# Performance work log

Measured on AMD Instinct MI355X. Metric: run time of the kernel, lower is better.

The kernel has to match this reference:

```python
import jax, jax.numpy as jnp
import numpy as np

G, S, P = 128, 32, 16          # graphs, subgraphs per graph, nodes per subgraph
D, C, NH, OUT = 768, 256, 4, 7 # input dim, hidden dim, GAT heads, classes


def setup_inputs() -> dict:
    key = jax.random.key(0)
    ks = jax.random.split(key, 17)
    n = lambda k, shape, s=0.05: jax.random.normal(k, shape, dtype=jnp.float32) * s
    return {
        "x": jax.random.normal(ks[0], (G, S, P, D), dtype=jnp.float32),
        # GATConv(768 -> 256, heads=4, concat=False): lin weight, att vectors, bias
        "gat_W": n(ks[1], (D, NH * C)),
        "att_src": n(ks[2], (NH, C)),
        "att_dst": n(ks[3], (NH, C)),
        "gat_b": n(ks[4], (C,)),
        # GRU(256 -> 256), torch layout [3*H, in]
        "gru_Wih": n(ks[5], (3 * C, C)),
        "gru_Whh": n(ks[6], (3 * C, C)),
        "gru_bih": n(ks[7], (3 * C,)),
        "gru_bhh": n(ks[8], (3 * C,)),
        # scale_up_projection Linear(256 -> 768)
        "up_W": n(ks[9], (D, C)),
        "up_b": n(ks[10], (D,)),
        # speaker_projection Linear(1536 -> 768) + ReLU
        "sp_W": n(ks[11], (D, 2 * D)),
        "sp_b": n(ks[12], (D,)),
        # GlobalAttention gate Linear(256 -> 1)
        "att_W": n(ks[13], (1, C)),
        "att_b": n(ks[14], (1,)),
        # classifier Linear(256 -> 7)
        "cls_W": n(ks[15], (OUT, C)),
        "cls_b": n(ks[16], (OUT,)),
    }


def _gat(x, W, a_src, a_dst, b):
    # PyG GATConv on a star graph (speaker = local node 0 -> all others) with
    # default add_self_loops=True, negative_slope=0.2, concat=False (mean over heads).
    # x: [G, P, D]
    h = jnp.einsum('gpd,dhc->gphc', x, W.reshape(D, NH, C))     # per-head transform
    es = jnp.sum(h * a_src, -1)                                 # [G, P, NH]
    ed = jnp.sum(h * a_dst, -1)
    lrelu = lambda v: jnp.where(v > 0, v, 0.2 * v)
    e_spk = lrelu(es[:, :1] + ed)   # edge speaker -> t
    e_slf = lrelu(es + ed)          # self loop t -> t
    w = jax.nn.softmax(jnp.stack([e_spk, e_slf], -1), axis=-1)  # [G, P, NH, 2]
    # for t == 0 both terms are h[:,0] and weights sum to 1, matching the
    # speaker node receiving only its self loop.
    out = w[..., 0:1] * h[:, :1] + w[..., 1:2] * h              # [G, P, NH, C]
    return out.mean(axis=2) + b


def _gru_cell(xin, h, Wih, Whh, bih, bhh):
    gi = xin @ Wih.T + bih
    gh = h @ Whh.T + bhh
    ir, iz, inn = jnp.split(gi, 3, -1)
    hr, hz, hn = jnp.split(gh, 3, -1)
    r = jax.nn.sigmoid(ir + hr)
    z = jax.nn.sigmoid(iz + hz)
    return (1 - z) * jnp.tanh(inn + r * hn) + z * h


def _forward(x, gat_W, att_src, att_dst, gat_b, gru_Wih, gru_Whh, gru_bih, gru_bhh,
             up_W, up_b, sp_W, sp_b, att_W, att_b, cls_W, cls_b):
    g, s, p, d = x.shape
    m0 = _gat(x[:, 0], gat_W, att_src, att_dst, gat_b)  # [G, P, C]
    h0 = jnp.zeros((g, p, C), x.dtype)

    def step(carry, _):
        h_run, m_prev = carry
        # running GRU hidden over memory prefix, then one zero-input step
        # (equivalent to rerunning the GRU over [m_0..m_{j-1}, 0])
        h_run = _gru_cell(m_prev, h_run, gru_Wih, gru_Whh, gru_bih, gru_bhh)
        h_nxt = _gru_cell(jnp.zeros_like(h_run), h_run, gru_Wih, gru_Whh, gru_bih, gru_bhh)
        pooled = h_nxt @ up_W.T + up_b                  # [G, P, D]
        # faithful to source: non_speaker_indices covers ALL nodes (torch.equal
        # shape-mismatch bug), and speaker_info is read AFTER the overwrite,
        # so the speaker concat is [pooled, pooled] and raw x[:, j>=1] is unused.
        spk = jnp.concatenate([pooled[:, 0], pooled[:, 0]], -1)  # [G, 2D]
        spk = jax.nn.relu(spk @ sp_W.T + sp_b)
        x_new = pooled.at[:, 0].set(spk)
        m = _gat(x_new, gat_W, att_src, att_dst, gat_b)
        return (h_run, m), m

    (_, _), ms = jax.lax.scan(step, (h0, m0), None, length=s - 1)
    mem = jnp.concatenate([m0[None], ms], axis=0)        # [S, G, P, C]
    # GlobalAttention pool over the P nodes of each subgraph memory state
    gate = jax.nn.softmax(jnp.squeeze(mem @ att_W.T + att_b, -1), axis=-1)  # [S, G, P]
    pooled = jnp.einsum('sgp,sgpc->sgc', gate, mem)
    logits = pooled @ cls_W.T + cls_b                    # [S, G, OUT]
    # torch stacks graph-major: [G*S, 1, OUT]
    return jnp.transpose(logits, (1, 0, 2)).reshape(g * s, 1, OUT)


def reference(x, gat_W, att_src, att_dst, gat_b, gru_Wih, gru_Whh, gru_bih, gru_bhh,
              up_W, up_b, sp_W, sp_b, att_W, att_b, cls_W, cls_b):
    return _forward(x, gat_W, att_src, att_dst, gat_b, gru_Wih, gru_Whh, gru_bih,
                    gru_bhh, up_W, up_b, sp_W, sp_b, att_W, att_b, cls_W, cls_b)
```

## Files before the change

kernel.cpp:

```cpp
#include <hip/hip_runtime.h>
#include <math.h>

#define NG 128
#define NS 32
#define NP 16
#define ND 768
#define NC 256
#define NHD 4
#define NOUT 7
#define NR 2048

typedef unsigned short ushortT;
typedef short bf16x8 __attribute__((ext_vector_type(8)));
typedef float f32x4 __attribute__((ext_vector_type(4)));

__device__ __forceinline__ ushortT f2b(float f) {
    union { float f; unsigned u; } v; v.f = f;
    unsigned r = (v.u + 0x7FFF + ((v.u >> 16) & 1)) >> 16;
    return (ushortT)r;
}
__device__ __forceinline__ float sigf(float v) { return 1.f / (1.f + expf(-v)); }

#define MFMA16(a, b, c) __builtin_amdgcn_mfma_f32_16x16x32_bf16((a), (b), (c), 0, 0, 0)

__global__ __launch_bounds__(256) void bgemm_kernel(
    const ushortT* __restrict__ A, const ushortT* __restrict__ Asub,
    const ushortT* __restrict__ Bt, const float* __restrict__ bias,
    float* __restrict__ outF, ushortT* __restrict__ outH,
    int N, int K, int act)
{
    __shared__ short As[64 * 40];
    __shared__ short Bs[64 * 40];
    const int tid = threadIdx.x;
    const int lane = tid & 63, wid = tid >> 6;
    const int quad = lane >> 4, l15 = lane & 15;
    const int row0 = blockIdx.y * 64, col0 = blockIdx.x * 64;
    const int mh = (wid & 1) * 32, nh = (wid >> 1) * 32;
    const int sr = tid >> 2, skq = (tid & 3) * 8;
    const int grow_s = row0 + sr;
    const ushortT* aptr = (Asub && ((grow_s & 15) == 0))
        ? Asub + (size_t)(grow_s >> 4) * K : A + (size_t)grow_s * K;
    const ushortT* bptr = Bt + (size_t)(col0 + sr) * K;

    f32x4 acc[2][2];
    for (int i = 0; i < 2; ++i)
        for (int j = 0; j < 2; ++j) acc[i][j] = (f32x4){0.f, 0.f, 0.f, 0.f};

    for (int kk = 0; kk < K; kk += 32) {
        __syncthreads();
        *(uint4*)&As[sr * 40 + skq] = *(const uint4*)(aptr + kk + skq);
        *(uint4*)&Bs[sr * 40 + skq] = *(const uint4*)(bptr + kk + skq);
        __syncthreads();
        bf16x8 af0 = *(const bf16x8*)&As[(mh + l15) * 40 + quad * 8];
        bf16x8 af1 = *(const bf16x8*)&As[(mh + 16 + l15) * 40 + quad * 8];
        bf16x8 bf0 = *(const bf16x8*)&Bs[(nh + l15) * 40 + quad * 8];
        bf16x8 bf1 = *(const bf16x8*)&Bs[(nh + 16 + l15) * 40 + quad * 8];
        acc[0][0] = MFMA16(af0, bf0, acc[0][0]);
        acc[0][1] = MFMA16(af0, bf1, acc[0][1]);
        acc[1][0] = MFMA16(af1, bf0, acc[1][0]);
        acc[1][1] = MFMA16(af1, bf1, acc[1][1]);
    }
#pragma unroll
    for (int mt = 0; mt < 2; ++mt)
#pragma unroll
        for (int nt = 0; nt < 2; ++nt) {
            const int gc = col0 + nh + nt * 16 + l15;
            const float bv = bias ? bias[gc] : 0.f;
#pragma unroll
            for (int r = 0; r < 4; ++r) {
                const int gr = row0 + mh + mt * 16 + quad * 4 + r;
                float v = acc[mt][nt][r] + bv;
                if (act) v = fmaxf(v, 0.f);
                if (outF) outF[(size_t)gr * N + gc] = v;
                if (outH) outH[(size_t)gr * N + gc] = f2b(v);
            }
        }
}

__global__ __launch_bounds__(256) void gru1_mfma_kernel(
    const ushortT* __restrict__ mB, const ushortT* __restrict__ hB,
    const ushortT* __restrict__ WihB, const ushortT* __restrict__ WhhB,
    const float* __restrict__ bih, const float* __restrict__ bhh,
    float* __restrict__ hF, ushortT* __restrict__ hBout)
{
    __shared__ short As[2 * 32 * 264];
    __shared__ short Bs[384 * 40];
    const int tid = threadIdx.x;
    const int lane = tid & 63, wid = tid >> 6;
    const int quad = lane >> 4, l15 = lane & 15;
    const int row0 = blockIdx.y * 32;
    const int n0 = blockIdx.x * 64;
    const int mt = wid & 1, nhh = (wid >> 1) * 32;

    for (int c = tid; c < 2048; c += 256) {
        const int mat = c >> 10, r2 = c & 1023, row = r2 >> 5, kc = (r2 & 31) * 8;
        const ushortT* src = (mat ? hB : mB) + (size_t)(row0 + row) * NC + kc;
        *(uint4*)&As[mat * 8448 + row * 264 + kc] = *(const uint4*)src;
    }
    f32x4 acc[2][3][2];
    for (int w = 0; w < 2; ++w)
        for (int g = 0; g < 3; ++g)
            for (int n = 0; n < 2; ++n) acc[w][g][n] = (f32x4){0.f, 0.f, 0.f, 0.f};

    for (int kk = 0; kk < 256; kk += 32) {
        __syncthreads();
        for (int c = tid; c < 1536; c += 256) {
            const int j = c >> 2, kq = (c & 3) * 8;
            const int w = j / 192, j2 = j - w * 192, gt = j2 >> 6, nloc = j2 & 63;
            const ushortT* src = (w ? WhhB : WihB) +
                (size_t)(gt * 256 + n0 + nloc) * NC + kk + kq;
            *(uint4*)&Bs[j * 40 + kq] = *(const uint4*)src;
        }
        __syncthreads();
        bf16x8 af0 = *(const bf16x8*)&As[(mt * 16 + l15) * 264 + kk + quad * 8];
        bf16x8 af1 = *(const bf16x8*)&As[8448 + (mt * 16 + l15) * 264 + kk + quad * 8];
#pragma unroll
        for (int gt = 0; gt < 3; ++gt)
#pragma unroll
            for (int nt = 0; nt < 2; ++nt) {
                const int jb = gt * 64 + nhh + nt * 16 + l15;
                bf16x8 b0 = *(const bf16x8*)&Bs[jb * 40 + quad * 8];
                bf16x8 b1 = *(const bf16x8*)&Bs[(192 + jb) * 40 + quad * 8];
                acc[0][gt][nt] = MFMA16(af0, b0, acc[0][gt][nt]);
                acc[1][gt][nt] = MFMA16(af1, b1, acc[1][gt][nt]);
            }
    }
#pragma unroll
    for (int nt = 0; nt < 2; ++nt) {
        const int c = n0 + nhh + nt * 16 + l15;
        const float br = bih[c], bz = bih[256 + c], bn = bih[512 + c];
        const float cr = bhh[c], cz = bhh[256 + c], cn = bhh[512 + c];
#pragma unroll
        for (int r = 0; r < 4; ++r) {
            const int grow = row0 + mt * 16 + quad * 4 + r;
            const size_t idx = (size_t)grow * NC + c;
            const float hold = hF[idx];
            const float rg = sigf(acc[0][0][nt][r] + br + acc[1][0][nt][r] + cr);
            const float zg = sigf(acc[0][1][nt][r] + bz + acc[1][1][nt][r] + cz);
            const float ng = tanhf(acc[0][2][nt][r] + bn + rg * (acc[1][2][nt][r] + cn));
            const float hn = (1.f - zg) * ng + zg * hold;
            hF[idx] = hn;
            hBout[idx] = f2b(hn);
        }
    }
}

__global__ __launch_bounds__(256) void gru2_mfma_kernel(
    const ushortT* __restrict__ hB, const ushortT* __restrict__ WhhB,
    const float* __restrict__ bih, const float* __restrict__ bhh,
    const float* __restrict__ hF, ushortT* __restrict__ hnB,
    ushortT* __restrict__ h0c)
{
    __shared__ short As[32 * 264];
    __shared__ short Bs[192 * 40];
    const int tid = threadIdx.x;
    const int lane = tid & 63, wid = tid >> 6;
    const int quad = lane >> 4, l15 = lane & 15;
    const int row0 = blockIdx.y * 32;
    const int n0 = blockIdx.x * 64;
    const int mt = wid & 1, nhh = (wid >> 1) * 32;

    for (int c = tid; c < 1024; c += 256) {
        const int row = c >> 5, kc = (c & 31) * 8;
        *(uint4*)&As[row * 264 + kc] =
            *(const uint4*)(hB + (size_t)(row0 + row) * NC + kc);
    }
    f32x4 acc[3][2];
    for (int g = 0; g < 3; ++g)
        for (int n = 0; n < 2; ++n) acc[g][n] = (f32x4){0.f, 0.f, 0.f, 0.f};

    for (int kk = 0; kk < 256; kk += 32) {
        __syncthreads();
        for (int c = tid; c < 768; c += 256) {
            const int j = c >> 2, kq = (c & 3) * 8;
            const int gt = j >> 6, nloc = j & 63;
            *(uint4*)&Bs[j * 40 + kq] =
                *(const uint4*)(WhhB + (size_t)(gt * 256 + n0 + nloc) * NC + kk + kq);
        }
        __syncthreads();
        bf16x8 af = *(const bf16x8*)&As[(mt * 16 + l15) * 264 + kk + quad * 8];
#pragma unroll
        for (int gt = 0; gt < 3; ++gt)
#pragma unroll
            for (int nt = 0; nt < 2; ++nt) {
                const int jb = gt * 64 + nhh + nt * 16 + l15;
                bf16x8 b = *(const bf16x8*)&Bs[jb * 40 + quad * 8];
                acc[gt][nt] = MFMA16(af, b, acc[gt][nt]);
            }
    }
#pragma unroll
    for (int nt = 0; nt < 2; ++nt) {
        const int c = n0 + nhh + nt * 16 + l15;
        const float br = bih[c], bz = bih[256 + c], bn = bih[512 + c];
        const float cr = bhh[c], cz = bhh[256 + c], cn = bhh[512 + c];
#pragma unroll
        for (int r = 0; r < 4; ++r) {
            const int grow = row0 + mt * 16 + quad * 4 + r;
            const size_t idx = (size_t)grow * NC + c;
            const float rg = sigf(br + acc[0][nt][r] + cr);
            const float zg = sigf(bz + acc[1][nt][r] + cz);
            const float ng = tanhf(bn + rg * (acc[2][nt][r] + cn));
            const float hv = (1.f - zg) * ng + zg * hF[idx];
            const ushortT hb = f2b(hv);
            hnB[idx] = hb;
            if ((grow & 15) == 0) h0c[(size_t)(grow >> 4) * NC + c] = hb;
        }
    }
}

__global__ __launch_bounds__(256) void fin_kernel(
    const float* __restrict__ hbuf, const float* __restrict__ att_src,
    const float* __restrict__ att_dst, const float* __restrict__ gat_b,
    const float* __restrict__ attW, const float* __restrict__ attb,
    const float* __restrict__ clsW, const float* __restrict__ clsb,
    ushortT* __restrict__ mB, float* __restrict__ outp, int s)
{
    const int g = blockIdx.x, tid = threadIdx.x;
    const int lane = tid & 63, wid = tid >> 6;
    __shared__ float es_s[16][4], ed_s[16][4];
    __shared__ float m_s[16][260];
    __shared__ float gate_s[16];
    __shared__ float pooled_s[256];
    const float* hb = hbuf + (size_t)g * NP * (NHD * NC);

    for (int pi = 0; pi < 4; ++pi) {
        const int p = wid * 4 + pi;
        const float* row = hb + p * (NHD * NC);
        float ss[4] = {0.f, 0.f, 0.f, 0.f}, sd[4] = {0.f, 0.f, 0.f, 0.f};
#pragma unroll
        for (int i = 0; i < 16; ++i) {
            const int col = lane + 64 * i;
            const float v = row[col];
            ss[i >> 2] += v * att_src[col];
            sd[i >> 2] += v * att_dst[col];
        }
        for (int off = 32; off; off >>= 1)
#pragma unroll
            for (int h = 0; h < 4; ++h) {
                ss[h] += __shfl_down(ss[h], off);
                sd[h] += __shfl_down(sd[h], off);
            }
        if (lane == 0)
#pragma unroll
            for (int h = 0; h < 4; ++h) { es_s[p][h] = ss[h]; ed_s[p][h] = sd[h]; }
    }
    __syncthreads();
    {
        const int p = tid >> 4, cb = (tid & 15) * 16;
        float accv[16];
#pragma unroll
        for (int cj = 0; cj < 16; ++cj) accv[cj] = 0.f;
#pragma unroll
        for (int h = 0; h < 4; ++h) {
            float e1 = es_s[0][h] + ed_s[p][h]; e1 = e1 > 0.f ? e1 : 0.2f * e1;
            float e2 = es_s[p][h] + ed_s[p][h]; e2 = e2 > 0.f ? e2 : 0.2f * e2;
            const float mx = fmaxf(e1, e2);
            float w0 = expf(e1 - mx), w1 = expf(e2 - mx);
            const float inv = 1.f / (w0 + w1);
            w0 *= inv; w1 *= inv;
            const float* r0 = hb + h * NC + cb;
            const float* rp = hb + p * (NHD * NC) + h * NC + cb;
#pragma unroll
            for (int cj = 0; cj < 16; ++cj) accv[cj] += w0 * r0[cj] + w1 * rp[cj];
        }
#pragma unroll
        for (int cj = 0; cj < 16; ++cj) {
            const float v = accv[cj] * 0.25f + gat_b[cb + cj];
            m_s[p][cb + cj] = v;
            mB[(size_t)(g * NP + p) * NC + cb + cj] = f2b(v);
        }
    }
    __syncthreads();
    for (int pi = 0; pi < 4; ++pi) {
        const int p = wid * 4 + pi;
        float sg = 0.f;
#pragma unroll
        for (int i = 0; i < 4; ++i) { const int c = lane + 64 * i; sg += m_s[p][c] * attW[c]; }
        for (int off = 32; off; off >>= 1) sg += __shfl_down(sg, off);
        if (lane == 0) gate_s[p] = sg + attb[0];
    }
    __syncthreads();
    float mx = -1e30f;
#pragma unroll
    for (int p = 0; p < 16; ++p) mx = fmaxf(mx, gate_s[p]);
    float ge[16], ssum = 0.f;
#pragma unroll
    for (int p = 0; p < 16; ++p) { ge[p] = expf(gate_s[p] - mx); ssum += ge[p]; }
    const float inv = 1.f / ssum;
    {
        float pc = 0.f;
#pragma unroll
        for (int p = 0; p < 16; ++p) pc += ge[p] * m_s[p][tid];
        pooled_s[tid] = pc * inv;
    }
    __syncthreads();
    const int o = tid >> 5, l32 = tid & 31;
    if (o < NOUT) {
        float a = 0.f;
#pragma unroll
        for (int i = 0; i < 8; ++i) {
            const int c = l32 + 32 * i;
            a += pooled_s[c] * clsW[o * NC + c];
        }
        for (int off = 16; off; off >>= 1) a += __shfl_down(a, off);
        if (l32 == 0) outp[((size_t)g * NS + s) * NOUT + o] = a + clsb[o];
    }
}

__global__ __launch_bounds__(256) void cast_kernel(const float* __restrict__ a,
                                                   ushortT* __restrict__ b, int n) {
    const int i = blockIdx.x * 256 + threadIdx.x;
    if (i < n) b[i] = f2b(a[i]);
}
__global__ __launch_bounds__(256) void gatT_kernel(const float* __restrict__ gW,
                                                   ushortT* __restrict__ gB) {
    const int idx = blockIdx.x * 256 + threadIdx.x;
    const int c = idx / ND, d = idx - c * ND;
    gB[idx] = f2b(gW[(size_t)d * (NHD * NC) + c]);
}
__global__ __launch_bounds__(256) void spwc_kernel(const float* __restrict__ spW,
                                                   float* __restrict__ o) {
    const int idx = blockIdx.x * 256 + threadIdx.x;
    const int r = idx / ND, d = idx - r * ND;
    o[idx] = spW[(size_t)r * (2 * ND) + d] + spW[(size_t)r * (2 * ND) + ND + d];
}
__global__ __launch_bounds__(256) void wus_kernel(const float* __restrict__ spWc,
                                                  const float* __restrict__ upW,
                                                  ushortT* __restrict__ WusB) {
    const int c = threadIdx.x;
    const int o0 = blockIdx.x * 16;
    float acc[16];
#pragma unroll
    for (int i = 0; i < 16; ++i) acc[i] = 0.f;
    for (int d = 0; d < ND; ++d) {
        const float u = upW[(size_t)d * NC + c];
#pragma unroll
        for (int i = 0; i < 16; ++i) acc[i] += spWc[(size_t)(o0 + i) * ND + d] * u;
    }
#pragma unroll
    for (int i = 0; i < 16; ++i) WusB[(size_t)(o0 + i) * NC + c] = f2b(acc[i]);
}
__global__ __launch_bounds__(256) void bus_kernel(const float* __restrict__ spWc,
                                                  const float* __restrict__ up_b,
                                                  const float* __restrict__ sp_b,
                                                  float* __restrict__ bus) {
    const int o = blockIdx.x * 256 + threadIdx.x;
    if (o >= ND) return;
    float a = sp_b[o];
    const float* sr = spWc + (size_t)o * ND;
    for (int d = 0; d < ND; ++d) a += sr[d] * up_b[d];
    bus[o] = a;
}
__global__ __launch_bounds__(256) void x0_kernel(const float* __restrict__ x,
                                                 ushortT* __restrict__ xb) {
    const int idx = blockIdx.x * 256 + threadIdx.x;
    const int row = idx / ND, d = idx - row * ND;
    const int g = row >> 4, p = row & 15;
    xb[idx] = f2b(x[((size_t)g * (NS * NP) + p) * ND + d]);
}
__global__ __launch_bounds__(256) void zh_kernel(float* hF, ushortT* hB) {
    const int idx = blockIdx.x * 256 + threadIdx.x;
    hF[idx] = 0.f;
    hB[idx] = 0;
}

extern "C" void kernel_launch(void* const* d_in, const int* in_sizes, int n_in,
                              void* d_out, int out_size, void* d_ws, size_t ws_size,
                              hipStream_t stream) {
    (void)in_sizes; (void)n_in; (void)out_size; (void)ws_size;
    const float* x       = (const float*)d_in[0];
    const float* gat_W   = (const float*)d_in[1];
    const float* att_src = (const float*)d_in[2];
    const float* att_dst = (const float*)d_in[3];
    const float* gat_b   = (const float*)d_in[4];
    const float* gru_Wih = (const float*)d_in[5];
    const float* gru_Whh = (const float*)d_in[6];
    const float* gru_bih = (const float*)d_in[7];
    const float* gru_bhh = (const float*)d_in[8];
    const float* up_W    = (const float*)d_in[9];
    const float* up_b    = (const float*)d_in[10];
    const float* sp_W    = (const float*)d_in[11];
    const float* sp_b    = (const float*)d_in[12];
    const float* att_W   = (const float*)d_in[13];
    const float* att_b   = (const float*)d_in[14];
    const float* cls_W   = (const float*)d_in[15];
    const float* cls_b   = (const float*)d_in[16];
    float* outp = (float*)d_out;

    char* w = (char*)d_ws;
    ushortT* xb    = (ushortT*)w; w += (size_t)NR * ND * 2;
    ushortT* WihB  = (ushortT*)w; w += (size_t)(3 * NC) * NC * 2;
    ushortT* WhhB  = (ushortT*)w; w += (size_t)(3 * NC) * NC * 2;
    ushortT* upWB  = (ushortT*)w; w += (size_t)ND * NC * 2;
    ushortT* gatB  = (ushortT*)w; w += (size_t)(NHD * NC) * ND * 2;
    ushortT* WusB  = (ushortT*)w; w += (size_t)ND * NC * 2;
    float*   spWc  = (float*)w;   w += (size_t)ND * ND * 4;
    float*   bus   = (float*)w;   w += (size_t)ND * 4;
    float*   hF    = (float*)w;   w += (size_t)NR * NC * 4;
    ushortT* hB    = (ushortT*)w; w += (size_t)NR * NC * 2;
    ushortT* hnB   = (ushortT*)w; w += (size_t)NR * NC * 2;
    ushortT* h0c   = (ushortT*)w; w += (size_t)NG * NC * 2;
    ushortT* poolB = (ushortT*)w; w += (size_t)NR * ND * 2;
    ushortT* spkB  = (ushortT*)w; w += (size_t)NG * ND * 2;
    float*   hbuf  = (float*)w;   w += (size_t)NR * (NHD * NC) * 4;
    ushortT* mB    = (ushortT*)w; w += (size_t)NR * NC * 2;

    cast_kernel<<<768, 256, 0, stream>>>(gru_Wih, WihB, 3 * NC * NC);
    cast_kernel<<<768, 256, 0, stream>>>(gru_Whh, WhhB, 3 * NC * NC);
    cast_kernel<<<768, 256, 0, stream>>>(up_W, upWB, ND * NC);
    gatT_kernel<<<(NHD * NC * ND) / 256, 256, 0, stream>>>(gat_W, gatB);
    spwc_kernel<<<(ND * ND) / 256, 256, 0, stream>>>(sp_W, spWc);
    wus_kernel<<<ND / 16, 256, 0, stream>>>(spWc, up_W, WusB);
    bus_kernel<<<3, 256, 0, stream>>>(spWc, up_b, sp_b, bus);
    x0_kernel<<<(NR * ND) / 256, 256, 0, stream>>>(x, xb);
    zh_kernel<<<(NR * NC) / 256, 256, 0, stream>>>(hF, hB);

    bgemm_kernel<<<dim3((NHD * NC) / 64, NR / 64), 256, 0, stream>>>(
        xb, nullptr, gatB, nullptr, hbuf, nullptr, NHD * NC, ND, 0);
    fin_kernel<<<NG, 256, 0, stream>>>(hbuf, att_src, att_dst, gat_b,
                                       att_W, att_b, cls_W, cls_b, mB, outp, 0);

    for (int j = 1; j < NS; ++j) {
        gru1_mfma_kernel<<<dim3(NC / 64, NR / 32), 256, 0, stream>>>(
            mB, hB, WihB, WhhB, gru_bih, gru_bhh, hF, hB);
        gru2_mfma_kernel<<<dim3(NC / 64, NR / 32), 256, 0, stream>>>(
            hB, WhhB, gru_bih, gru_bhh, hF, hnB, h0c);
        bgemm_kernel<<<dim3(ND / 64, NR / 64), 256, 0, stream>>>(
            hnB, nullptr, upWB, up_b, nullptr, poolB, ND, NC, 0);
        bgemm_kernel<<<dim3(ND / 64, NG / 64), 256, 0, stream>>>(
            h0c, nullptr, WusB, bus, nullptr, spkB, ND, NC, 1);
        bgemm_kernel<<<dim3((NHD * NC) / 64, NR / 64), 256, 0, stream>>>(
            poolB, spkB, gatB, nullptr, hbuf, nullptr, NHD * NC, ND, 0);
        fin_kernel<<<NG, 256, 0, stream>>>(hbuf, att_src, att_dst, gat_b,
                                           att_W, att_b, cls_W, cls_b, mB, outp, j);
    }
}
```

Measured before the change: 2.644 ms.

## Fold up-projection into GAT weight and fuse per-step GEMMs with GAT finish

Precomputes a combined up_W·gat_W weight and bias so the per-step 256→768→1024 chain becomes one 256→1024 GEMM. That GEMM is fused into a per-graph kernel that also does the attention and classifier steps. A separate small kernel computes the speaker path (speaker projection plus GAT transform) for the node-0 rows. This cuts per-step launches from six to four and removes the 768-wide intermediate poolB and the fp32 hbuf round trips, at the cost of a different rounding order (bf16 folded weights) and only 128 blocks per fused kernel.

```diff
diff --git a/kernel.cpp b/kernel.cpp
--- a/kernel.cpp
+++ b/kernel.cpp
@@ -19,15 +19,17 @@
     unsigned r = (v.u + 0x7FFF + ((v.u >> 16) & 1)) >> 16;
     return (ushortT)r;
 }
+__device__ __forceinline__ float b2f(ushortT u) {
+    union { unsigned u; float f; } v; v.u = ((unsigned)u) << 16; return v.f;
+}
 __device__ __forceinline__ float sigf(float v) { return 1.f / (1.f + expf(-v)); }
 
 #define MFMA16(a, b, c) __builtin_amdgcn_mfma_f32_16x16x32_bf16((a), (b), (c), 0, 0, 0)
 
 __global__ __launch_bounds__(256) void bgemm_kernel(
-    const ushortT* __restrict__ A, const ushortT* __restrict__ Asub,
-    const ushortT* __restrict__ Bt, const float* __restrict__ bias,
-    float* __restrict__ outF, ushortT* __restrict__ outH,
-    int N, int K, int act)
+    const ushortT* __restrict__ A, const ushortT* __restrict__ Bt,
+    const float* __restrict__ bias, float* __restrict__ outF,
+    ushortT* __restrict__ outH, int N, int K, int act)
 {
     __shared__ short As[64 * 40];
     __shared__ short Bs[64 * 40];
@@ -37,9 +39,7 @@
     const int row0 = blockIdx.y * 64, col0 = blockIdx.x * 64;
     const int mh = (wid & 1) * 32, nh = (wid >> 1) * 32;
     const int sr = tid >> 2, skq = (tid & 3) * 8;
-    const int grow_s = row0 + sr;
-    const ushortT* aptr = (Asub && ((grow_s & 15) == 0))
-        ? Asub + (size_t)(grow_s >> 4) * K : A + (size_t)grow_s * K;
+    const ushortT* aptr = A + (size_t)(row0 + sr) * K;
     const ushortT* bptr = Bt + (size_t)(col0 + sr) * K;
 
     f32x4 acc[2][2];
@@ -208,6 +208,200 @@
     }
 }
 
+__global__ __launch_bounds__(256) void spkgat_kernel(
+    const ushortT* __restrict__ h0c, const ushortT* __restrict__ WusB,
+    const float* __restrict__ bus, const ushortT* __restrict__ gatB,
+    ushortT* __restrict__ hs)
+{
+    __shared__ short h0s[16 * 264];
+    __shared__ short spks[16 * 776];
+    const int tid = threadIdx.x;
+    const int lane = tid & 63, wid = tid >> 6;
+    const int quad = lane >> 4, l15 = lane & 15;
+    const int rows0 = blockIdx.y * 16, cols0 = blockIdx.x * 128;
+
+    for (int c = tid; c < 512; c += 256) {
+        const int row = c >> 5, kc = (c & 31) * 8;
+        *(uint4*)&h0s[row * 264 + kc] =
+            *(const uint4*)(h0c + (size_t)(rows0 + row) * NC + kc);
+    }
+    __syncthreads();
+    f32x4 accA[12];
+    for (int t = 0; t < 12; ++t) accA[t] = (f32x4){0.f, 0.f, 0.f, 0.f};
+    for (int kk = 0; kk < NC; kk += 32) {
+        bf16x8 af = *(const bf16x8*)&h0s[l15 * 264 + kk + quad * 8];
+#pragma unroll
+        for (int t = 0; t < 12; ++t) {
+            const int col = wid * 192 + t * 16 + l15;
+            bf16x8 b = *(const bf16x8*)(WusB + (size_t)col * NC + kk + quad * 8);
+            accA[t] = MFMA16(af, b, accA[t]);
+        }
+    }
+#pragma unroll
+    for (int t = 0; t < 12; ++t) {
+        const int col = wid * 192 + t * 16 + l15;
+        const float bv = bus[col];
+#pragma unroll
+        for (int r = 0; r < 4; ++r) {
+            float v = accA[t][r] + bv;
+            v = fmaxf(v, 0.f);
+            spks[(quad * 4 + r) * 776 + col] = f2b(v);
+        }
+    }
+    __syncthreads();
+    f32x4 accB[2];
+    accB[0] = (f32x4){0.f, 0.f, 0.f, 0.f};
+    accB[1] = (f32x4){0.f, 0.f, 0.f, 0.f};
+    for (int kk = 0; kk < ND; kk += 32) {
+        bf16x8 af = *(const bf16x8*)&spks[l15 * 776 + kk + quad * 8];
+#pragma unroll
+        for (int t = 0; t < 2; ++t) {
+            const int col = cols0 + wid * 32 + t * 16 + l15;
+            bf16x8 b = *(const bf16x8*)(gatB + (size_t)col * ND + kk + quad * 8);
+            accB[t] = MFMA16(af, b, accB[t]);
+        }
+    }
+#pragma unroll
+    for (int t = 0; t < 2; ++t) {
+        const int col = cols0 + wid * 32 + t * 16 + l15;
+#pragma unroll
+        for (int r = 0; r < 4; ++r)
+            hs[(size_t)(rows0 + quad * 4 + r) * 1024 + col] = f2b(accB[t][r]);
+    }
+}
+
+__global__ __launch_bounds__(256) void gatfin_kernel(
+    const ushortT* __restrict__ hnB, const ushortT* __restrict__ hs,
+    const ushortT* __restrict__ WugT, const float* __restrict__ bug,
+    const float* __restrict__ att_src, const float* __restrict__ att_dst,
+    const float* __restrict__ gat_b, const float* __restrict__ attW,
+    const float* __restrict__ attb, const float* __restrict__ clsW,
+    const float* __restrict__ clsb, ushortT* __restrict__ mB,
+    float* __restrict__ outp, int s)
+{
+    const int g = blockIdx.x, tid = threadIdx.x;
+    const int lane = tid & 63, wid = tid >> 6;
+    const int quad = lane >> 4, l15 = lane & 15;
+    __shared__ short hn_s[16 * 264];
+    __shared__ ushortT hb_s[16][1040];
+    __shared__ float es_s[16][4], ed_s[16][4];
+    __shared__ float m_s[16][260];
+    __shared__ float gate_s[16];
+    __shared__ float pooled_s[256];
+
+    for (int c = tid; c < 512; c += 256) {
+        const int row = c >> 5, kc = (c & 31) * 8;
+        *(uint4*)&hn_s[row * 264 + kc] =
+            *(const uint4*)(hnB + (size_t)(g * NP + row) * NC + kc);
+    }
+    __syncthreads();
+    f32x4 acc[16];
+#pragma unroll
+    for (int t = 0; t < 16; ++t) acc[t] = (f32x4){0.f, 0.f, 0.f, 0.f};
+    for (int kk = 0; kk < NC; kk += 32) {
+        bf16x8 af = *(const bf16x8*)&hn_s[l15 * 264 + kk + quad * 8];
+#pragma unroll
+        for (int t = 0; t < 16; ++t) {
+            const int col = wid * 256 + t * 16 + l15;
+            bf16x8 b = *(const bf16x8*)(WugT + (size_t)col * NC + kk + quad * 8);
+            acc[t] = MFMA16(af, b, acc[t]);
+        }
+    }
+#pragma unroll
+    for (int t = 0; t < 16; ++t) {
+        const int col = wid * 256 + t * 16 + l15;
+        const float bv = bug[col];
+#pragma unroll
+        for (int r = 0; r < 4; ++r)
+            hb_s[quad * 4 + r][col] = f2b(acc[t][r] + bv);
+    }
+    __syncthreads();
+    for (int c = tid; c < 1024; c += 256) hb_s[0][c] = hs[(size_t)g * 1024 + c];
+    __syncthreads();
+
+    for (int pi = 0; pi < 4; ++pi) {
+        const int p = wid * 4 + pi;
+        float ss[4] = {0.f, 0.f, 0.f, 0.f}, sd[4] = {0.f, 0.f, 0.f, 0.f};
+#pragma unroll
+        for (int i = 0; i < 16; ++i) {
+            const int col = lane + 64 * i;
+            const float v = b2f(hb_s[p][col]);
+            ss[i >> 2] += v * att_src[col];
+            sd[i >> 2] += v * att_dst[col];
+        }
+        for (int off = 32; off; off >>= 1)
+#pragma unroll
+            for (int h = 0; h < 4; ++h) {
+                ss[h] += __shfl_down(ss[h], off);
+                sd[h] += __shfl_down(sd[h], off);
+            }
+        if (lane == 0)
+#pragma unroll
+            for (int h = 0; h < 4; ++h) { es_s[p][h] = ss[h]; ed_s[p][h] = sd[h]; }
+    }
+    __syncthreads();
+    {
+        const int p = tid >> 4, cb = (tid & 15) * 16;
+        float accv[16];
+#pragma unroll
+        for (int cj = 0; cj < 16; ++cj) accv[cj] = 0.f;
+#pragma unroll
+        for (int h = 0; h < 4; ++h) {
+            float e1 = es_s[0][h] + ed_s[p][h]; e1 = e1 > 0.f ? e1 : 0.2f * e1;
+            float e2 = es_s[p][h] + ed_s[p][h]; e2 = e2 > 0.f ? e2 : 0.2f * e2;
+            const float mx = fmaxf(e1, e2);
+            float w0 = expf(e1 - mx), w1 = expf(e2 - mx);
+            const float inv = 1.f / (w0 + w1);
+            w0 *= inv; w1 *= inv;
+#pragma unroll
+            for (int cj = 0; cj < 16; ++cj)
+                accv[cj] += w0 * b2f(hb_s[0][h * NC + cb + cj])
+                          + w1 * b2f(hb_s[p][h * NC + cb + cj]);
+        }
+#pragma unroll
+        for (int cj = 0; cj < 16; ++cj) {
+            const float v = accv[cj] * 0.25f + gat_b[cb + cj];
+            m_s[p][cb + cj] = v;
+            mB[(size_t)(g * NP + p) * NC + cb + cj] = f2b(v);
+        }
+    }
+    __syncthreads();
+    for (int pi = 0; pi < 4; ++pi) {
+        const int p = wid * 4 + pi;
+        float sg = 0.f;
+#pragma unroll
+        for (int i = 0; i < 4; ++i) { const int c = lane + 64 * i; sg += m_s[p][c] * attW[c]; }
+        for (int off = 32; off; off >>= 1) sg += __shfl_down(sg, off);
+        if (lane == 0) gate_s[p] = sg + attb[0];
+    }
+    __syncthreads();
+    float mx = -1e30f;
+#pragma unroll
+    for (int p = 0; p < 16; ++p) mx = fmaxf(mx, gate_s[p]);
+    float ge[16], ssum = 0.f;
+#pragma unroll
+    for (int p = 0; p < 16; ++p) { ge[p] = expf(gate_s[p] - mx); ssum += ge[p]; }
+    const float inv = 1.f / ssum;
+    {
+        float pc = 0.f;
+#pragma unroll
+        for (int p = 0; p < 16; ++p) pc += ge[p] * m_s[p][tid];
+        pooled_s[tid] = pc * inv;
+    }
+    __syncthreads();
+    const int o = tid >> 5, l32 = tid & 31;
+    if (o < NOUT) {
+        float a = 0.f;
+#pragma unroll
+        for (int i = 0; i < 8; ++i) {
+            const int c = l32 + 32 * i;
+            a += pooled_s[c] * clsW[o * NC + c];
+        }
+        for (int off = 16; off; off >>= 1) a += __shfl_down(a, off);
+        if (l32 == 0) outp[((size_t)g * NS + s) * NOUT + o] = a + clsb[o];
+    }
+}
+
 __global__ __launch_bounds__(256) void fin_kernel(
     const float* __restrict__ hbuf, const float* __restrict__ att_src,
     const float* __restrict__ att_dst, const float* __restrict__ gat_b,
@@ -350,6 +544,21 @@
     const float* sr = spWc + (size_t)o * ND;
     for (int d = 0; d < ND; ++d) a += sr[d] * up_b[d];
     bus[o] = a;
+}
+__global__ __launch_bounds__(256) void upTc_kernel(const float* __restrict__ upW,
+                                                   ushortT* __restrict__ o) {
+    const int idx = blockIdx.x * 256 + threadIdx.x;
+    if (idx >= NC * ND) return;
+    const int c = idx / ND, d = idx - c * ND;
+    o[idx] = f2b(upW[(size_t)d * NC + c]);
+}
+__global__ __launch_bounds__(256) void bug_kernel(const float* __restrict__ gatW,
+                                                  const float* __restrict__ up_b,
+                                                  float* __restrict__ bug) {
+    const int col = blockIdx.x * 256 + threadIdx.x;
+    float a = 0.f;
+    for (int d = 0; d < ND; ++d) a += up_b[d] * gatW[(size_t)d * (NHD * NC) + col];
+    bug[col] = a;
 }
 __global__ __launch_bounds__(256) void x0_kernel(const float* __restrict__ x,
                                                  ushortT* __restrict__ xb) {
@@ -391,32 +600,36 @@
     ushortT* xb    = (ushortT*)w; w += (size_t)NR * ND * 2;
     ushortT* WihB  = (ushortT*)w; w += (size_t)(3 * NC) * NC * 2;
     ushortT* WhhB  = (ushortT*)w; w += (size_t)(3 * NC) * NC * 2;
-    ushortT* upWB  = (ushortT*)w; w += (size_t)ND * NC * 2;
     ushortT* gatB  = (ushortT*)w; w += (size_t)(NHD * NC) * ND * 2;
     ushortT* WusB  = (ushortT*)w; w += (size_t)ND * NC * 2;
+    ushortT* upWTc = (ushortT*)w; w += (size_t)NC * ND * 2;
+    ushortT* WugT  = (ushortT*)w; w += (size_t)(NHD * NC) * NC * 2;
     float*   spWc  = (float*)w;   w += (size_t)ND * ND * 4;
     float*   bus   = (float*)w;   w += (size_t)ND * 4;
+    float*   bug   = (float*)w;   w += (size_t)(NHD * NC) * 4;
     float*   hF    = (float*)w;   w += (size_t)NR * NC * 4;
     ushortT* hB    = (ushortT*)w; w += (size_t)NR * NC * 2;
     ushortT* hnB   = (ushortT*)w; w += (size_t)NR * NC * 2;
     ushortT* h0c   = (ushortT*)w; w += (size_t)NG * NC * 2;
-    ushortT* poolB = (ushortT*)w; w += (size_t)NR * ND * 2;
-    ushortT* spkB  = (ushortT*)w; w += (size_t)NG * ND * 2;
+    ushortT* hs    = (ushortT*)w; w += (size_t)NG * (NHD * NC) * 2;
     float*   hbuf  = (float*)w;   w += (size_t)NR * (NHD * NC) * 4;
     ushortT* mB    = (ushortT*)w; w += (size_t)NR * NC * 2;
 
     cast_kernel<<<768, 256, 0, stream>>>(gru_Wih, WihB, 3 * NC * NC);
     cast_kernel<<<768, 256, 0, stream>>>(gru_Whh, WhhB, 3 * NC * NC);
-    cast_kernel<<<768, 256, 0, stream>>>(up_W, upWB, ND * NC);
     gatT_kernel<<<(NHD * NC * ND) / 256, 256, 0, stream>>>(gat_W, gatB);
     spwc_kernel<<<(ND * ND) / 256, 256, 0, stream>>>(sp_W, spWc);
     wus_kernel<<<ND / 16, 256, 0, stream>>>(spWc, up_W, WusB);
     bus_kernel<<<3, 256, 0, stream>>>(spWc, up_b, sp_b, bus);
+    upTc_kernel<<<(NC * ND) / 256, 256, 0, stream>>>(up_W, upWTc);
+    bgemm_kernel<<<dim3(NC / 64, (NHD * NC) / 64), 256, 0, stream>>>(
+        gatB, upWTc, nullptr, nullptr, WugT, NC, ND, 0);
+    bug_kernel<<<4, 256, 0, stream>>>(gat_W, up_b, bug);
     x0_kernel<<<(NR * ND) / 256, 256, 0, stream>>>(x, xb);
     zh_kernel<<<(NR * NC) / 256, 256, 0, stream>>>(hF, hB);
 
     bgemm_kernel<<<dim3((NHD * NC) / 64, NR / 64), 256, 0, stream>>>(
-        xb, nullptr, gatB, nullptr, hbuf, nullptr, NHD * NC, ND, 0);
+        xb, gatB, nullptr, hbuf, nullptr, NHD * NC, ND, 0);
     fin_kernel<<<NG, 256, 0, stream>>>(hbuf, att_src, att_dst, gat_b,
                                        att_W, att_b, cls_W, cls_b, mB, outp, 0);
 
@@ -425,13 +638,9 @@
             mB, hB, WihB, WhhB, gru_bih, gru_bhh, hF, hB);
         gru2_mfma_kernel<<<dim3(NC / 64, NR / 32), 256, 0, stream>>>(
             hB, WhhB, gru_bih, gru_bhh, hF, hnB, h0c);
-        bgemm_kernel<<<dim3(ND / 64, NR / 64), 256, 0, stream>>>(
-            hnB, nullptr, upWB, up_b, nullptr, poolB, ND, NC, 0);
-        bgemm_kernel<<<dim3(ND / 64, NG / 64), 256, 0, stream>>>(
-            h0c, nullptr, WusB, bus, nullptr, spkB, ND, NC, 1);
-        bgemm_kernel<<<dim3((NHD * NC) / 64, NR / 64), 256, 0, stream>>>(
-            poolB, spkB, gatB, nullptr, hbuf, nullptr, NHD * NC, ND, 0);
-        fin_kernel<<<NG, 256, 0, stream>>>(hbuf, att_src, att_dst, gat_b,
-                                           att_W, att_b, cls_W, cls_b, mB, outp, j);
-    }
-}
+        spkgat_kernel<<<dim3(8, 8), 256, 0, stream>>>(h0c, WusB, bus, gatB, hs);
+        gatfin_kernel<<<NG, 256, 0, stream>>>(hnB, hs, WugT, bug,
+                                              att_src, att_dst, gat_b, att_W,
+                                              att_b, cls_W, cls_b, mB, outp, j);
+    }
+}
```

Measured after the change: 2.756 ms. +4.2%, slower.
